# Optimization experiments

Measured on AMD Instinct MI355X. Metric: run time of the kernel, lower is better.

## Reference

```python
import jax, jax.numpy as jnp
import numpy as np

KMAX = 16


def setup_inputs() -> dict:
    key = jax.random.key(0)
    k1, k2, k3 = jax.random.split(key, 3)
    B, S, D = 8, 2048, 128
    first_point = jax.random.normal(k1, (B, S, 3), dtype=jnp.float32)
    first_index = jnp.sort(
        jax.random.randint(k2, (B, S, 1), 0, 20000, dtype=jnp.int64), axis=1
    )
    attribute = jax.random.normal(k3, (B, S, D), dtype=jnp.float32)
    return {"first_point": first_point, "first_index": first_index, "attribute": attribute}


def _pairwise_sqdist(p):
    # p: [B, S, 3] -> [B, S, S]; loop over the 3 coordinate dims like the
    # original to avoid a [B, S, S, 3] intermediate.
    d2 = (p[..., 0][:, :, None] - p[..., 0][:, None, :]) ** 2
    for n in range(1, 3):
        d2 = d2 + (p[..., n][:, :, None] - p[..., n][:, None, :]) ** 2
    return d2


def reference(first_point, first_index, attribute):
    B, S, _ = first_point.shape
    # squared pairwise distances (squared=True branch)
    d2 = _pairwise_sqdist(first_point)                      # [B, S, S]
    # K nearest neighbors via full argsort (faithful to torch.argsort[:, :, :K])
    neighbors = jnp.argsort(d2, axis=-1)[:, :, :KMAX]       # [B, S, K]

    b_idx = jnp.arange(B)[:, None, None]                    # [B, 1, 1]

    # gather attributes of neighbors: [B, S, K, D]
    attr_nb = attribute[b_idx, neighbors]

    # 'distance' coordinate: gathered squared distances -> [B, S, K, 1]
    distance_neighbors = jnp.take_along_axis(d2, neighbors, axis=-1)[..., None]

    # 'index_distance' coordinate: |first_index - neighbor_index| -> [B, S, K, 1]
    nei_index = first_index[b_idx, neighbors]               # [B, S, K, 1]
    index_distance = jnp.abs(
        (first_index[:, :, None, :] - nei_index).astype(jnp.float32)
    )

    return (distance_neighbors, index_distance, attr_nb)
```

## Files before the change

kernel.cpp:

```cpp
#include <hip/hip_runtime.h>

#define NB 8
#define NS 2048
#define ND 128
#define NK 16

typedef float f32x4 __attribute__((ext_vector_type(4)));

template <int KIND>
__device__ inline int partner_i32(int v) {
    if constexpr (KIND == 1) {
        return __builtin_amdgcn_update_dpp(0, v, 0xB1, 0xF, 0xF, true);
    } else if constexpr (KIND == 2) {
        return __builtin_amdgcn_update_dpp(0, v, 0x4E, 0xF, 0xF, true);
    } else if constexpr (KIND == 32) {
        return __shfl_xor(v, 32, 64);
    } else {
        constexpr int imm = (KIND << 10) | 0x1F;
        return __builtin_amdgcn_ds_swizzle(v, imm);
    }
}
template <int KIND>
__device__ inline float partner_f32(float v) {
    return __int_as_float(partner_i32<KIND>(__float_as_int(v)));
}
template <int KIND>
__device__ inline double partner_f64(double v) {
    const long long x = __double_as_longlong(v);
    const int lo = partner_i32<KIND>((int)(unsigned int)x);
    const int hi = partner_i32<KIND>((int)(x >> 32));
    return __longlong_as_double(((long long)hi << 32) | (unsigned int)lo);
}
__device__ inline float partner_f32_dyn(float v, int d) {
    switch (d) {
    case 1:  return partner_f32<1>(v);
    case 2:  return partner_f32<2>(v);
    case 4:  return partner_f32<4>(v);
    case 8:  return partner_f32<8>(v);
    case 16: return partner_f32<16>(v);
    default: return partner_f32<32>(v);
    }
}
__device__ inline double partner_f64_dyn(double v, int d) {
    switch (d) {
    case 1:  return partner_f64<1>(v);
    case 2:  return partner_f64<2>(v);
    case 4:  return partner_f64<4>(v);
    case 8:  return partner_f64<8>(v);
    case 16: return partner_f64<16>(v);
    default: return partner_f64<32>(v);
    }
}
__device__ inline double shfl_idx_f64(double v, int src) {
    const long long x = __double_as_longlong(v);
    const int lo = __shfl((int)(unsigned int)x, src, 64);
    const int hi = __shfl((int)(x >> 32), src, 64);
    return __longlong_as_double(((long long)hi << 32) | (unsigned int)lo);
}

__device__ inline float bitonic_sort64_f32(float v, int lane) {
#pragma unroll
    for (int k = 2; k <= 64; k <<= 1) {
#pragma unroll
        for (int d = k >> 1; d >= 1; d >>= 1) {
            const float o = partner_f32_dyn(v, d);
            const float mn = fminf(v, o);
            const float mx = fmaxf(v, o);
            const bool keepMin = ((lane & k) == 0) == ((lane & d) == 0);
            v = keepMin ? mn : mx;
        }
    }
    return v;
}
__device__ inline double bitonic_sort64_f64(double v, int lane) {
#pragma unroll
    for (int k = 2; k <= 64; k <<= 1) {
#pragma unroll
        for (int d = k >> 1; d >= 1; d >>= 1) {
            const double o = partner_f64_dyn(v, d);
            const double mn = fmin(v, o);
            const double mx = fmax(v, o);
            const bool keepMin = ((lane & k) == 0) == ((lane & d) == 0);
            v = keepMin ? mn : mx;
        }
    }
    return v;
}

__global__ __launch_bounds__(256) void knn_kernel(
    const float* __restrict__ pts,
    const int*   __restrict__ fidx,
    const float* __restrict__ attr,
    float*       __restrict__ out)
{
    __shared__ float spts[NS * 3];
    __shared__ double sbuf[4][66];

    const int tid  = threadIdx.x;
    const int wv   = tid >> 6;
    const int lane = tid & 63;
    const int row  = blockIdx.x * 4 + wv;
    const int b = row >> 11;
    const int i = row & 2047;

    {
        const f32x4* src = (const f32x4*)(pts + (size_t)b * NS * 3);
        f32x4* dst = (f32x4*)spts;
#pragma unroll
        for (int k = 0; k < 6; ++k) dst[k * 256 + tid] = src[k * 256 + tid];
    }
    __syncthreads();

    const float qx = spts[i * 3 + 0];
    const float qy = spts[i * 3 + 1];
    const float qz = spts[i * 3 + 2];

    float dist[32];
    float m = 3.4e38f;
#pragma unroll
    for (int t = 0; t < 32; ++t) {
        const int j = t * 64 + lane;
        const float x = spts[j * 3 + 0];
        const float y = spts[j * 3 + 1];
        const float z = spts[j * 3 + 2];
        const float dx = __fsub_rn(qx, x);
        const float dy = __fsub_rn(qy, y);
        const float dz = __fsub_rn(qz, z);
        float d = __fmul_rn(dx, dx);
        d = __fadd_rn(d, __fmul_rn(dy, dy));
        d = __fadd_rn(d, __fmul_rn(dz, dz));
        dist[t] = d;
        m = fminf(m, d);
    }

    const float ms = bitonic_sort64_f32(m, lane);
    const float T = __shfl(ms, 15, 64);

    double* sw = &sbuf[wv][0];
    const double INF = __longlong_as_double(0x7FF0000000000000LL);
    double r = INF;
    for (int c0 = 0;; c0 += 64) {
        sw[lane] = INF;
        int base = 0;
#pragma unroll
        for (int t = 0; t < 32; ++t) {
            const bool pred = (dist[t] <= T);
            const unsigned long long bal = __ballot(pred);
            const int rank = __builtin_amdgcn_mbcnt_hi(
                (unsigned int)(bal >> 32),
                __builtin_amdgcn_mbcnt_lo((unsigned int)bal, 0));
            const int slot = base + rank;
            const bool inw = pred && ((unsigned int)(slot - c0) < 64u);
            const unsigned int hi = __float_as_uint(dist[t]) + 0x10000000u;
            const unsigned int lo = (unsigned int)(t * 64) | (unsigned int)lane;
            const double kd = __longlong_as_double(((long long)hi << 32) | lo);
            sw[inw ? (slot - c0) : 64] = kd;
            base += (int)__popcll(bal);
        }
        const int M = base;
        asm volatile("s_waitcnt lgkmcnt(0)" ::: "memory");
        double v = sw[lane];
        v = bitonic_sort64_f64(v, lane);
        if (c0 == 0) {
            r = v;
        } else {
            double s = shfl_idx_f64(v, (15 - lane) & 63);
            double ml = fmin(r, s);
#pragma unroll
            for (int d = 8; d >= 1; d >>= 1) {
                const double o = partner_f64_dyn(ml, d);
                const double mn = fmin(ml, o);
                const double mx = fmax(ml, o);
                ml = ((lane & d) == 0) ? mn : mx;
            }
            r = ml;
        }
        if (M <= c0 + 64) break;
    }

    const long long kb = __double_as_longlong(r);
    const int jsel = (int)(unsigned int)kb;
    const unsigned int db = (unsigned int)((unsigned long long)kb >> 32) - 0x10000000u;

    float* out0 = out;
    float* out1 = out + (size_t)NB * NS * NK;
    float* out2 = out + (size_t)2 * NB * NS * NK;
    const size_t rowBase = (size_t)row * NK;

    if (lane < NK) {
        out0[rowBase + lane] = __uint_as_float(db);
        const int ii = fidx[(size_t)b * NS + i];
        const int jj = fidx[(size_t)b * NS + jsel];
        out1[rowBase + lane] = fabsf((float)(ii - jj));
    }

    const int half = lane >> 5;
    const int comp = lane & 31;
    const float* ab = attr + (size_t)b * NS * ND;
    float* o2row = out2 + rowBase * ND;

    int jj8[8];
#pragma unroll
    for (int p = 0; p < 8; ++p) jj8[p] = __shfl(jsel, 2 * p + half, 64);
    f32x4 v8[8];
#pragma unroll
    for (int p = 0; p < 8; ++p)
        v8[p] = *(const f32x4*)(ab + (size_t)jj8[p] * ND + comp * 4);
#pragma unroll
    for (int p = 0; p < 8; ++p)
        *(f32x4*)(o2row + (size_t)(2 * p + half) * ND + comp * 4) = v8[p];
}

extern "C" void kernel_launch(void* const* d_in, const int* in_sizes, int n_in,
                              void* d_out, int out_size, void* d_ws, size_t ws_size,
                              hipStream_t stream) {
    const float* pts  = (const float*)d_in[0];
    const int*   fidx = (const int*)d_in[1];
    const float* attr = (const float*)d_in[2];
    float* out = (float*)d_out;

    const int rows = NB * NS;
    const int blocks = rows / 4;
    knn_kernel<<<blocks, 256, 0, stream>>>(pts, fidx, attr, out);
}
```

Baseline: 40.39 us.

## Use SoA swizzled shared points, contiguous per-lane candidates, and 32-wide candidate sort

Shared memory now holds points in structure-of-arrays form with an XOR swizzle, so each lane reads its 32 contiguous candidates as vectorized f32x4 loads without bank conflicts. Candidate indices become lane*32+u instead of t*64+lane. The per-chunk candidate buffer shrinks from 64 to 32 entries and uses a 32-wide bitonic sort, which cuts shuffle stages. An occupancy hint of 6 blocks per SM is added. The tradeoffs are a strided global load during staging, and more merge iterations when more than 32 candidates tie under the threshold.

New measurement: 62.42 us. 54.5% more time.

```diff
diff --git a/kernel.cpp b/kernel.cpp
--- a/kernel.cpp
+++ b/kernel.cpp
@@ -47,8 +47,7 @@
     case 2:  return partner_f64<2>(v);
     case 4:  return partner_f64<4>(v);
     case 8:  return partner_f64<8>(v);
-    case 16: return partner_f64<16>(v);
-    default: return partner_f64<32>(v);
+    default: return partner_f64<16>(v);
     }
 }
 __device__ inline double shfl_idx_f64(double v, int src) {
@@ -72,9 +71,10 @@
     }
     return v;
 }
-__device__ inline double bitonic_sort64_f64(double v, int lane) {
-#pragma unroll
-    for (int k = 2; k <= 64; k <<= 1) {
+
+__device__ inline double bitonic_sort32_f64(double v, int lane) {
+#pragma unroll
+    for (int k = 2; k <= 32; k <<= 1) {
 #pragma unroll
         for (int d = k >> 1; d >= 1; d >>= 1) {
             const double o = partner_f64_dyn(v, d);
@@ -87,14 +87,19 @@
     return v;
 }
 
-__global__ __launch_bounds__(256) void knn_kernel(
+__device__ inline int swz(int j) {
+    const int u = j & 31;
+    return (j & ~31) | ((((u >> 2) ^ ((j >> 5) & 7)) << 2) | (u & 3));
+}
+
+__global__ __launch_bounds__(256, 6) void knn_kernel(
     const float* __restrict__ pts,
     const int*   __restrict__ fidx,
     const float* __restrict__ attr,
     float*       __restrict__ out)
 {
-    __shared__ float spts[NS * 3];
-    __shared__ double sbuf[4][66];
+    __shared__ __align__(16) float sp[3 * NS];
+    __shared__ double sbuf[4][32];
 
     const int tid  = threadIdx.x;
     const int wv   = tid >> 6;
@@ -104,33 +109,46 @@
     const int i = row & 2047;
 
     {
-        const f32x4* src = (const f32x4*)(pts + (size_t)b * NS * 3);
-        f32x4* dst = (f32x4*)spts;
-#pragma unroll
-        for (int k = 0; k < 6; ++k) dst[k * 256 + tid] = src[k * 256 + tid];
+        const float* pb = pts + (size_t)b * NS * 3;
+#pragma unroll
+        for (int p = 0; p < 8; ++p) {
+            const int j = p * 256 + tid;
+            const float x = pb[j * 3 + 0];
+            const float y = pb[j * 3 + 1];
+            const float z = pb[j * 3 + 2];
+            const int w = swz(j);
+            sp[w] = x;
+            sp[NS + w] = y;
+            sp[2 * NS + w] = z;
+        }
     }
     __syncthreads();
 
-    const float qx = spts[i * 3 + 0];
-    const float qy = spts[i * 3 + 1];
-    const float qz = spts[i * 3 + 2];
+    const int wi = swz(i);
+    const float qx = sp[wi];
+    const float qy = sp[NS + wi];
+    const float qz = sp[2 * NS + wi];
 
     float dist[32];
     float m = 3.4e38f;
-#pragma unroll
-    for (int t = 0; t < 32; ++t) {
-        const int j = t * 64 + lane;
-        const float x = spts[j * 3 + 0];
-        const float y = spts[j * 3 + 1];
-        const float z = spts[j * 3 + 2];
-        const float dx = __fsub_rn(qx, x);
-        const float dy = __fsub_rn(qy, y);
-        const float dz = __fsub_rn(qz, z);
-        float d = __fmul_rn(dx, dx);
-        d = __fadd_rn(d, __fmul_rn(dy, dy));
-        d = __fadd_rn(d, __fmul_rn(dz, dz));
-        dist[t] = d;
-        m = fminf(m, d);
+    const int base = lane * 32;
+#pragma unroll
+    for (int c = 0; c < 8; ++c) {
+        const int slot = base + (((c ^ (lane & 7)) << 2));
+        const f32x4 X = *(const f32x4*)&sp[slot];
+        const f32x4 Y = *(const f32x4*)&sp[NS + slot];
+        const f32x4 Z = *(const f32x4*)&sp[2 * NS + slot];
+#pragma unroll
+        for (int k = 0; k < 4; ++k) {
+            const float dx = __fsub_rn(qx, X[k]);
+            const float dy = __fsub_rn(qy, Y[k]);
+            const float dz = __fsub_rn(qz, Z[k]);
+            float d = __fmul_rn(dx, dx);
+            d = __fadd_rn(d, __fmul_rn(dy, dy));
+            d = __fadd_rn(d, __fmul_rn(dz, dz));
+            dist[c * 4 + k] = d;
+            m = fminf(m, d);
+        }
     }
 
     const float ms = bitonic_sort64_f32(m, lane);
@@ -139,28 +157,27 @@
     double* sw = &sbuf[wv][0];
     const double INF = __longlong_as_double(0x7FF0000000000000LL);
     double r = INF;
-    for (int c0 = 0;; c0 += 64) {
-        sw[lane] = INF;
-        int base = 0;
-#pragma unroll
-        for (int t = 0; t < 32; ++t) {
-            const bool pred = (dist[t] <= T);
+    for (int c0 = 0;; c0 += 32) {
+        if (lane < 32) sw[lane] = INF;
+        int cnt = 0;
+#pragma unroll
+        for (int u = 0; u < 32; ++u) {
+            const bool pred = (dist[u] <= T);
             const unsigned long long bal = __ballot(pred);
             const int rank = __builtin_amdgcn_mbcnt_hi(
                 (unsigned int)(bal >> 32),
                 __builtin_amdgcn_mbcnt_lo((unsigned int)bal, 0));
-            const int slot = base + rank;
-            const bool inw = pred && ((unsigned int)(slot - c0) < 64u);
-            const unsigned int hi = __float_as_uint(dist[t]) + 0x10000000u;
-            const unsigned int lo = (unsigned int)(t * 64) | (unsigned int)lane;
-            const double kd = __longlong_as_double(((long long)hi << 32) | lo);
-            sw[inw ? (slot - c0) : 64] = kd;
-            base += (int)__popcll(bal);
-        }
-        const int M = base;
+            const int slot = cnt + rank - c0;
+            if (pred && (unsigned int)slot < 32u) {
+                const unsigned int hi = __float_as_uint(dist[u]) + 0x10000000u;
+                const unsigned int lo = (unsigned int)(base + u);
+                sw[slot] = __longlong_as_double(((long long)hi << 32) | lo);
+            }
+            cnt += (int)__popcll(bal);
+        }
         asm volatile("s_waitcnt lgkmcnt(0)" ::: "memory");
-        double v = sw[lane];
-        v = bitonic_sort64_f64(v, lane);
+        double v = sw[lane & 31];
+        v = bitonic_sort32_f64(v, lane);
         if (c0 == 0) {
             r = v;
         } else {
@@ -175,7 +192,7 @@
             }
             r = ml;
         }
-        if (M <= c0 + 64) break;
+        if (cnt <= c0 + 32) break;
     }
 
     const long long kb = __double_as_longlong(r);
```
